# Performance work log

Hardware: AMD Instinct MI355X
Metric: run time of the kernel (lower is better)

The kernel has to match this reference:

```python
import jax, jax.numpy as jnp
import numpy as np

GRID_SIZE = 8
SPLINE_ORDER = 3  # cubic B-splines
GRID_MIN, GRID_MAX = -1.0, 1.0


def _make_grid():
    # Extended knot vector: grid_size + 2*order intervals -> G+2k+1 knots
    h = (GRID_MAX - GRID_MIN) / GRID_SIZE
    n = GRID_SIZE + 2 * SPLINE_ORDER + 1
    return jnp.asarray(GRID_MIN - SPLINE_ORDER * h + h * np.arange(n, dtype=np.float32))


def bspline_basis(x, grid, k):
    # x: (B, in) -> (B, in, G+k) via Cox-de Boor recursion
    x = x[..., None]
    b = ((x >= grid[:-1]) & (x < grid[1:])).astype(x.dtype)
    for p in range(1, k + 1):
        left = (x - grid[: -(p + 1)]) / (grid[p:-1] - grid[: -(p + 1)]) * b[..., :-1]
        right = (grid[p + 1:] - x) / (grid[p + 1:] - grid[1:-p]) * b[..., 1:]
        b = left + right
    return b


def setup_inputs() -> dict:
    key = jax.random.key(0)
    k1, k2, k3 = jax.random.split(key, 3)
    B, IN, OUT = 32768, 256, 256
    NB = GRID_SIZE + SPLINE_ORDER  # 11
    x = jax.random.normal(k1, (B, IN), dtype=jnp.float32)
    ln_gamma = jnp.ones((IN,), dtype=jnp.float32)
    ln_beta = jnp.zeros((IN,), dtype=jnp.float32)
    coeff = jax.random.normal(k2, (OUT, IN, NB), dtype=jnp.float32) * 0.1
    base_w = jax.random.normal(k3, (OUT, IN), dtype=jnp.float32) * (1.0 / np.sqrt(IN))
    return {"x": x, "ln_gamma": ln_gamma, "ln_beta": ln_beta, "coeff": coeff, "base_w": base_w}


def reference(x, ln_gamma, ln_beta, coeff, base_w):
    grid = _make_grid()
    # LayerNorm over in_features (eps = torch default 1e-5)
    mu = jnp.mean(x, axis=-1, keepdims=True)
    var = jnp.mean(jnp.square(x - mu), axis=-1, keepdims=True)
    normalized = (x - mu) * jax.lax.rsqrt(var + 1e-5) * ln_gamma + ln_beta
    # Spline branch: basis expansion (B, in, nb) contracted with coeff (out, in, nb)
    basis = bspline_basis(normalized, grid, SPLINE_ORDER)
    spline = jnp.einsum('bin,oin->bo', basis, coeff)
    # Base branch: SiLU(x) @ W^T (note: uses raw x, not normalized)
    base = jnp.einsum('bi,oi->bo', jax.nn.silu(x), base_w)
    return spline + base
```

## Files before the change

kernel.cpp:

```cpp
#include <hip/hip_runtime.h>
#include <hip/hip_bf16.h>

typedef _Float16 f16x8 __attribute__((ext_vector_type(8)));
typedef float f32x4 __attribute__((ext_vector_type(4)));

#define BM 128
#define NCHUNK 32
#define IN_F 256
#define OUT_F 256
#define KDIM 3072

__device__ inline void async_b16(const void* g, void* l) {
  __builtin_amdgcn_global_load_lds(
      (const __attribute__((address_space(1))) unsigned int*)g,
      (__attribute__((address_space(3))) unsigned int*)l, 16, 0, 0);
}

static __device__ inline unsigned pack2(float a, float b) {
  union { _Float16 h[2]; unsigned u; } t;
  t.h[0] = (_Float16)a;
  t.h[1] = (_Float16)b;
  return t.u;
}

__global__ __launch_bounds__(256) void prep_w(const float* __restrict__ coeff,
                                              const float* __restrict__ base_w,
                                              _Float16* __restrict__ W2F) {
  const int u   = blockIdx.x * 256 + threadIdx.x;
  const int c   = u / 3072;
  const int r   = u % 3072;
  const int bcb = r / 192;
  const int r2  = r % 192;
  const int g   = r2 / 64;
  const int ln  = r2 % 64;
  const int o   = bcb * 16 + (ln & 15);
  const int k8  = g * 4 + (ln >> 4);
  const int kh0 = c * 96 + k8 * 8;
  _Float16 h[8];
  #pragma unroll
  for (int e = 0; e < 8; ++e) {
    const int k = kh0 + e;
    const int i = k / 12, m = k % 12;
    const float v = (m == 11) ? base_w[o * IN_F + i] : coeff[(o * IN_F + i) * 11 + m];
    h[e] = (_Float16)v;
  }
  *(f16x8*)&W2F[(size_t)u * 8] = *(const f16x8*)h;
}

__global__ __launch_bounds__(1024, 4) void kan_fused(const float* __restrict__ x,
                                                     const float* __restrict__ gamma,
                                                     const float* __restrict__ beta,
                                                     const _Float16* __restrict__ W2F,
                                                     float* __restrict__ out) {
  __shared__ _Float16 A0[24 * 512], A1[24 * 512];
  __shared__ _Float16 B0[48 * 512], B1[48 * 512];
  __shared__ float mu_s[BM], rs_s[BM];

  const int tid  = threadIdx.x;
  const int lane = tid & 63;
  const int wid  = tid >> 6;
  const int row0 = blockIdx.x * BM;

  for (int rr = wid; rr < BM; rr += 16) {
    const float4 v = *(const float4*)(x + (size_t)(row0 + rr) * IN_F + lane * 4);
    float s  = v.x + v.y + v.z + v.w;
    float sq = v.x * v.x + v.y * v.y + v.z * v.z + v.w * v.w;
    #pragma unroll
    for (int off = 32; off >= 1; off >>= 1) {
      s  += __shfl_xor(s, off);
      sq += __shfl_xor(sq, off);
    }
    if (lane == 0) {
      const float mu  = s * (1.0f / 256.0f);
      const float var = sq * (1.0f / 256.0f) - mu * mu;
      mu_s[rr] = mu;
      rs_s[rr] = 1.0f / sqrtf(var + 1e-5f);
    }
  }
  __syncthreads();

  const bool isprod = (wid < 8);

  const int wr   = (wid >> 2) & 1;
  const int wc   = wid & 3;
  const int lrow = lane & 15;

  f32x4 acc[4][4] = {};

  const int plrow = tid & 15;
  const int pfq   = (tid >> 4) & 3;
  const int prb   = (tid >> 6) & 7;
  const int prow  = prb * 16 + plrow;
  const float mu = mu_s[prow], rs = rs_s[prow];
  const float* xrow = x + (size_t)(row0 + prow) * IN_F + pfq * 2;
  const float* grow = gamma + pfq * 2;
  const float* brow = beta + pfq * 2;

  int aoff0, aoff1, aoff2;
  {
    const int k80 = pfq * 3 + 0, k81 = pfq * 3 + 1, k82 = pfq * 3 + 2;
    aoff0 = (prb * 3 + (k80 >> 2)) * 512 + (k80 & 3) * 128 + plrow * 8;
    aoff1 = (prb * 3 + (k81 >> 2)) * 512 + (k81 & 3) * 128 + plrow * 8;
    aoff2 = (prb * 3 + (k82 >> 2)) * 512 + (k82 & 3) * 128 + plrow * 8;
  }

  const char* const wsrc = (const char*)W2F + (size_t)(wid & 7) * 6144 + (size_t)lane * 16;
  auto stageB = [&](int c, _Float16* Bb) {
    const char* gb = wsrc + (size_t)c * 49152;
    char* lb = (char*)Bb + (wid & 7) * 6144;
    #pragma unroll
    for (int j = 0; j < 6; ++j)
      async_b16(gb + j * 1024, lb + j * 1024);
  };

  auto produce = [&](_Float16* buf, float2 xv, float2 gv, float2 bv) {
    unsigned R[12];
    #pragma unroll
    for (int q = 0; q < 2; ++q) {
      const float xr = q ? xv.y : xv.x;
      const float gq = q ? gv.y : gv.x;
      const float bq = q ? bv.y : bv.x;
      const float n  = (xr - mu) * rs * gq + bq;
      const float v  = (n + 1.75f) * 4.0f;
      const float fj = floorf(v);
      const float u  = v - fj;
      const float u2 = u * u, u3 = u2 * u;
      const float w0 = (1.0f / 6.0f) * (1.0f - 3.0f * u + 3.0f * u2 - u3);
      const float w1 = (1.0f / 6.0f) * (3.0f * u3 - 6.0f * u2 + 4.0f);
      const float w2 = (1.0f / 6.0f) * (-3.0f * u3 + 3.0f * u2 + 3.0f * u + 1.0f);
      const float w3 = (1.0f / 6.0f) * u3;
      const unsigned W0 = pack2(w0, w1);
      const unsigned W1 = pack2(w2, w3);
      const int p    = (int)fj - 3;
      const bool odd = (p & 1);
      const unsigned v0 = odd ? (W0 << 16) : W0;
      const unsigned v1 = odd ? ((W0 >> 16) | (W1 << 16)) : W1;
      const unsigned v2 = odd ? (W1 >> 16) : 0u;
      const int s0 = (v >= 0.0f && v < 14.0f) ? (p >> 1) : 99;
      const int s1 = s0 + 1, s2 = s0 + 2;
      #pragma unroll
      for (int k = 0; k < 6; ++k) {
        unsigned r = (k == s0) ? v0 : 0u;
        r = (k == s1) ? v1 : r;
        r = (k == s2) ? v2 : r;
        R[q * 6 + k] = r;
      }
      const float sl = xr * __builtin_amdgcn_rcpf(1.0f + __expf(-xr));
      R[q * 6 + 5] = (R[q * 6 + 5] & 0x0000FFFFu) | pack2(0.0f, sl);
    }
    *(f16x8*)&buf[aoff0] = *(const f16x8*)&R[0];
    *(f16x8*)&buf[aoff1] = *(const f16x8*)&R[4];
    *(f16x8*)&buf[aoff2] = *(const f16x8*)&R[8];
  };

  auto domfma = [&](const _Float16* Ab, const _Float16* Bb) {
    #pragma unroll
    for (int fk = 0; fk < 3; ++fk) {
      f16x8 a[4], b[4];
      #pragma unroll
      for (int fm = 0; fm < 4; ++fm)
        a[fm] = *(const f16x8*)&Ab[((wr * 4 + fm) * 3 + fk) * 512 + lane * 8];
      #pragma unroll
      for (int fn = 0; fn < 4; ++fn)
        b[fn] = *(const f16x8*)&Bb[((wc * 4 + fn) * 3 + fk) * 512 + lane * 8];
      #pragma unroll
      for (int fm = 0; fm < 4; ++fm)
        #pragma unroll
        for (int fn = 0; fn < 4; ++fn)
          acc[fm][fn] = __builtin_amdgcn_mfma_f32_16x16x32_f16(a[fm], b[fn], acc[fm][fn], 0, 0, 0);
    }
  };

  float2 xv0 = {}, gv0 = {}, bv0 = {}, xv1 = {}, gv1 = {}, bv1 = {};
  if (isprod) {
    stageB(0, B0);
    xv0 = *(const float2*)(xrow);
    gv0 = *(const float2*)(grow);
    bv0 = *(const float2*)(brow);
    xv1 = *(const float2*)(xrow + 8);
    gv1 = *(const float2*)(grow + 8);
    bv1 = *(const float2*)(brow + 8);
    produce(A0, xv0, gv0, bv0);
  }
  __syncthreads();

  for (int c = 0; c < NCHUNK; c += 2) {
    const int cp2 = (c + 2 < NCHUNK) ? (c + 2) : (NCHUNK - 1);
    const int cp3 = (c + 3 < NCHUNK) ? (c + 3) : (NCHUNK - 1);
    if (isprod) {
      stageB(c + 1, B1);
      xv0 = *(const float2*)(xrow + cp2 * 8);
      gv0 = *(const float2*)(grow + cp2 * 8);
      bv0 = *(const float2*)(brow + cp2 * 8);
      produce(A1, xv1, gv1, bv1);
    } else {
      domfma(A0, B0);
    }
    __syncthreads();
    if (isprod) {
      if (c + 2 < NCHUNK) {
        stageB(cp2, B0);
        xv1 = *(const float2*)(xrow + cp3 * 8);
        gv1 = *(const float2*)(grow + cp3 * 8);
        bv1 = *(const float2*)(brow + cp3 * 8);
        produce(A0, xv0, gv0, bv0);
      }
    } else {
      domfma(A1, B1);
    }
    __syncthreads();
  }

  if (!isprod) {
    const int orow0 = row0 + wr * 64 + (lane >> 4) * 4;
    const int ocol0 = wc * 64 + lrow;
    #pragma unroll
    for (int fm = 0; fm < 4; ++fm)
      #pragma unroll
      for (int fn = 0; fn < 4; ++fn)
        #pragma unroll
        for (int r = 0; r < 4; ++r)
          out[(size_t)(orow0 + fm * 16 + r) * OUT_F + ocol0 + fn * 16] = acc[fm][fn][r];
  }
}

extern "C" void kernel_launch(void* const* d_in, const int* in_sizes, int n_in,
                              void* d_out, int out_size, void* d_ws, size_t ws_size,
                              hipStream_t stream) {
  const float* x      = (const float*)d_in[0];
  const float* gamma  = (const float*)d_in[1];
  const float* beta   = (const float*)d_in[2];
  const float* coeff  = (const float*)d_in[3];
  const float* base_w = (const float*)d_in[4];
  float* out = (float*)d_out;
  _Float16* W2F = (_Float16*)d_ws;

  prep_w<<<dim3(384), dim3(256), 0, stream>>>(coeff, base_w, W2F);
  kan_fused<<<dim3(32768 / BM), dim3(1024), 0, stream>>>(x, gamma, beta, W2F, out);
}
```

Measured before the change: 74.04 us.

## Load weight fragments directly from global into registers instead of LDS staging

Removes the LDS double buffers for the weight matrix and the async global-to-LDS copies. Consumer waves now load their B fragments straight from global memory (L2) into registers, software-pipelined one k-step ahead. This frees LDS and removes producer-side staging work, but each consumer wave now issues redundant global loads, since the two row-group waves fetch the same columns. Load latency is exposed to the MFMA loop and is only covered by the single-step prefetch.

```diff
diff --git a/kernel.cpp b/kernel.cpp
--- a/kernel.cpp
+++ b/kernel.cpp
@@ -9,12 +9,6 @@
 #define IN_F 256
 #define OUT_F 256
 #define KDIM 3072
-
-__device__ inline void async_b16(const void* g, void* l) {
-  __builtin_amdgcn_global_load_lds(
-      (const __attribute__((address_space(1))) unsigned int*)g,
-      (__attribute__((address_space(3))) unsigned int*)l, 16, 0, 0);
-}
 
 static __device__ inline unsigned pack2(float a, float b) {
   union { _Float16 h[2]; unsigned u; } t;
@@ -53,7 +47,6 @@
                                                      const _Float16* __restrict__ W2F,
                                                      float* __restrict__ out) {
   __shared__ _Float16 A0[24 * 512], A1[24 * 512];
-  __shared__ _Float16 B0[48 * 512], B1[48 * 512];
   __shared__ float mu_s[BM], rs_s[BM];
 
   const int tid  = threadIdx.x;
@@ -103,15 +96,6 @@
     aoff1 = (prb * 3 + (k81 >> 2)) * 512 + (k81 & 3) * 128 + plrow * 8;
     aoff2 = (prb * 3 + (k82 >> 2)) * 512 + (k82 & 3) * 128 + plrow * 8;
   }
-
-  const char* const wsrc = (const char*)W2F + (size_t)(wid & 7) * 6144 + (size_t)lane * 16;
-  auto stageB = [&](int c, _Float16* Bb) {
-    const char* gb = wsrc + (size_t)c * 49152;
-    char* lb = (char*)Bb + (wid & 7) * 6144;
-    #pragma unroll
-    for (int j = 0; j < 6; ++j)
-      async_b16(gb + j * 1024, lb + j * 1024);
-  };
 
   auto produce = [&](_Float16* buf, float2 xv, float2 gv, float2 bv) {
     unsigned R[12];
@@ -153,27 +137,30 @@
     *(f16x8*)&buf[aoff2] = *(const f16x8*)&R[8];
   };
 
-  auto domfma = [&](const _Float16* Ab, const _Float16* Bb) {
-    #pragma unroll
-    for (int fk = 0; fk < 3; ++fk) {
-      f16x8 a[4], b[4];
-      #pragma unroll
-      for (int fm = 0; fm < 4; ++fm)
-        a[fm] = *(const f16x8*)&Ab[((wr * 4 + fm) * 3 + fk) * 512 + lane * 8];
+  const char* const wbsrc = (const char*)W2F + (size_t)wc * 12288 + (size_t)lane * 16;
+  auto loadB4 = [&](int c, int fk, f16x8* b4) {
+    const char* gb = wbsrc + (size_t)c * 49152;
+    #pragma unroll
+    for (int fn = 0; fn < 4; ++fn)
+      b4[fn] = *(const f16x8*)(gb + (fn * 3 + fk) * 1024);
+  };
+  auto constage = [&](const _Float16* Ab, int fk, const f16x8* bcur,
+                      f16x8* bnx, int cl, int fkl) {
+    loadB4(cl, fkl, bnx);
+    f16x8 a[4];
+    #pragma unroll
+    for (int fm = 0; fm < 4; ++fm)
+      a[fm] = *(const f16x8*)&Ab[((wr * 4 + fm) * 3 + fk) * 512 + lane * 8];
+    #pragma unroll
+    for (int fm = 0; fm < 4; ++fm)
       #pragma unroll
       for (int fn = 0; fn < 4; ++fn)
-        b[fn] = *(const f16x8*)&Bb[((wc * 4 + fn) * 3 + fk) * 512 + lane * 8];
-      #pragma unroll
-      for (int fm = 0; fm < 4; ++fm)
-        #pragma unroll
-        for (int fn = 0; fn < 4; ++fn)
-          acc[fm][fn] = __builtin_amdgcn_mfma_f32_16x16x32_f16(a[fm], b[fn], acc[fm][fn], 0, 0, 0);
-    }
+        acc[fm][fn] = __builtin_amdgcn_mfma_f32_16x16x32_f16(a[fm], bcur[fn], acc[fm][fn], 0, 0, 0);
   };
 
   float2 xv0 = {}, gv0 = {}, bv0 = {}, xv1 = {}, gv1 = {}, bv1 = {};
+  f16x8 bX[4], bY[4];
   if (isprod) {
-    stageB(0, B0);
     xv0 = *(const float2*)(xrow);
     gv0 = *(const float2*)(grow);
     bv0 = *(const float2*)(brow);
@@ -181,32 +168,38 @@
     gv1 = *(const float2*)(grow + 8);
     bv1 = *(const float2*)(brow + 8);
     produce(A0, xv0, gv0, bv0);
+  } else {
+    loadB4(0, 0, bX);
   }
   __syncthreads();
 
   for (int c = 0; c < NCHUNK; c += 2) {
-    const int cp2 = (c + 2 < NCHUNK) ? (c + 2) : (NCHUNK - 1);
+    const int cn1 = (c + 1 < NCHUNK) ? (c + 1) : (NCHUNK - 1);
+    const int cn2 = (c + 2 < NCHUNK) ? (c + 2) : (NCHUNK - 1);
+    const int cp2 = cn2;
     const int cp3 = (c + 3 < NCHUNK) ? (c + 3) : (NCHUNK - 1);
     if (isprod) {
-      stageB(c + 1, B1);
       xv0 = *(const float2*)(xrow + cp2 * 8);
       gv0 = *(const float2*)(grow + cp2 * 8);
       bv0 = *(const float2*)(brow + cp2 * 8);
       produce(A1, xv1, gv1, bv1);
     } else {
-      domfma(A0, B0);
+      constage(A0, 0, bX, bY, c, 1);
+      constage(A0, 1, bY, bX, c, 2);
+      constage(A0, 2, bX, bY, cn1, 0);
     }
     __syncthreads();
     if (isprod) {
       if (c + 2 < NCHUNK) {
-        stageB(cp2, B0);
         xv1 = *(const float2*)(xrow + cp3 * 8);
         gv1 = *(const float2*)(grow + cp3 * 8);
         bv1 = *(const float2*)(brow + cp3 * 8);
         produce(A0, xv0, gv0, bv0);
       }
     } else {
-      domfma(A1, B1);
+      constage(A1, 0, bY, bX, c + 1, 1);
+      constage(A1, 1, bX, bY, c + 1, 2);
+      constage(A1, 2, bY, bX, cn2, 0);
     }
     __syncthreads();
   }
```

After: 116.8 us. 1.58x slower.

## Switch GEMM to 32x32x16 MFMA tiles with matching A/B LDS layouts

Applied to the files above, without the earlier changes.

Replaces the 16x16x32 f16 MFMA tiling (4x4 accumulators per wave) with 32x32x16 MFMA (2x2 accumulators of 16 floats). The weight prep kernel and the producer's A-tile LDS write offsets are reorganized to match the 32-row fragment layout, and the epilogue is rewritten for the new accumulator mapping. The aim is fewer LDS fragment loads per MFMA and better reuse per instruction. In exchange, the producer now writes A with split 8-byte stores, which may cause more LDS bank conflicts.

```diff
diff --git a/kernel.cpp b/kernel.cpp
--- a/kernel.cpp
+++ b/kernel.cpp
@@ -2,7 +2,8 @@
 #include <hip/hip_bf16.h>
 
 typedef _Float16 f16x8 __attribute__((ext_vector_type(8)));
-typedef float f32x4 __attribute__((ext_vector_type(4)));
+typedef float f32x16 __attribute__((ext_vector_type(16)));
+typedef unsigned u32x2 __attribute__((ext_vector_type(2)));
 
 #define BM 128
 #define NCHUNK 32
@@ -29,13 +30,12 @@
   const int u   = blockIdx.x * 256 + threadIdx.x;
   const int c   = u / 3072;
   const int r   = u % 3072;
-  const int bcb = r / 192;
-  const int r2  = r % 192;
-  const int g   = r2 / 64;
+  const int cb  = r / 384;
+  const int r2  = r % 384;
+  const int kg  = r2 / 64;
   const int ln  = r2 % 64;
-  const int o   = bcb * 16 + (ln & 15);
-  const int k8  = g * 4 + (ln >> 4);
-  const int kh0 = c * 96 + k8 * 8;
+  const int o   = cb * 32 + (ln & 31);
+  const int kh0 = c * 96 + kg * 16 + (ln >> 5) * 8;
   _Float16 h[8];
   #pragma unroll
   for (int e = 0; e < 8; ++e) {
@@ -61,8 +61,8 @@
   const int wid  = tid >> 6;
   const int row0 = blockIdx.x * BM;
 
-  for (int rr = wid; rr < BM; rr += 16) {
-    const float4 v = *(const float4*)(x + (size_t)(row0 + rr) * IN_F + lane * 4);
+  for (int rr0 = wid; rr0 < BM; rr0 += 16) {
+    const float4 v = *(const float4*)(x + (size_t)(row0 + rr0) * IN_F + lane * 4);
     float s  = v.x + v.y + v.z + v.w;
     float sq = v.x * v.x + v.y * v.y + v.z * v.z + v.w * v.w;
     #pragma unroll
@@ -73,8 +73,8 @@
     if (lane == 0) {
       const float mu  = s * (1.0f / 256.0f);
       const float var = sq * (1.0f / 256.0f) - mu * mu;
-      mu_s[rr] = mu;
-      rs_s[rr] = 1.0f / sqrtf(var + 1e-5f);
+      mu_s[rr0] = mu;
+      rs_s[rr0] = 1.0f / sqrtf(var + 1e-5f);
     }
   }
   __syncthreads();
@@ -83,9 +83,8 @@
 
   const int wr   = (wid >> 2) & 1;
   const int wc   = wid & 3;
-  const int lrow = lane & 15;
-
-  f32x4 acc[4][4] = {};
+
+  f32x16 acc[2][2] = {};
 
   const int plrow = tid & 15;
   const int pfq   = (tid >> 4) & 3;
@@ -96,12 +95,15 @@
   const float* grow = gamma + pfq * 2;
   const float* brow = beta + pfq * 2;
 
-  int aoff0, aoff1, aoff2;
+  const int rb  = prow >> 5, rr = prow & 31;
+  const int base3 = (pfq >> 1) * 3;
+  int o1, o2, o3, o4;
   {
-    const int k80 = pfq * 3 + 0, k81 = pfq * 3 + 1, k82 = pfq * 3 + 2;
-    aoff0 = (prb * 3 + (k80 >> 2)) * 512 + (k80 & 3) * 128 + plrow * 8;
-    aoff1 = (prb * 3 + (k81 >> 2)) * 512 + (k81 & 3) * 128 + plrow * 8;
-    aoff2 = (prb * 3 + (k82 >> 2)) * 512 + (k82 & 3) * 128 + plrow * 8;
+    const int g0 = (rb * 6 + base3) * 512 + rr * 8;
+    const int g1 = (rb * 6 + base3 + 1) * 512 + rr * 8;
+    const int g2 = (rb * 6 + base3 + 2) * 512 + rr * 8;
+    if (!(pfq & 1)) { o1 = g0; o2 = g0 + 256; o3 = o2 + 4; o4 = g1; }
+    else            { o1 = g1 + 256; o2 = g2; o3 = o2 + 4; o4 = g2 + 256; }
   }
 
   const char* const wsrc = (const char*)W2F + (size_t)(wid & 7) * 6144 + (size_t)lane * 16;
@@ -148,26 +150,27 @@
       const float sl = xr * __builtin_amdgcn_rcpf(1.0f + __expf(-xr));
       R[q * 6 + 5] = (R[q * 6 + 5] & 0x0000FFFFu) | pack2(0.0f, sl);
     }
-    *(f16x8*)&buf[aoff0] = *(const f16x8*)&R[0];
-    *(f16x8*)&buf[aoff1] = *(const f16x8*)&R[4];
-    *(f16x8*)&buf[aoff2] = *(const f16x8*)&R[8];
+    *(f16x8*)&buf[o1] = *(const f16x8*)&R[0];
+    *(u32x2*)&buf[o2] = *(const u32x2*)&R[4];
+    *(u32x2*)&buf[o3] = *(const u32x2*)&R[6];
+    *(f16x8*)&buf[o4] = *(const f16x8*)&R[8];
   };
 
   auto domfma = [&](const _Float16* Ab, const _Float16* Bb) {
     #pragma unroll
-    for (int fk = 0; fk < 3; ++fk) {
-      f16x8 a[4], b[4];
-      #pragma unroll
-      for (int fm = 0; fm < 4; ++fm)
-        a[fm] = *(const f16x8*)&Ab[((wr * 4 + fm) * 3 + fk) * 512 + lane * 8];
-      #pragma unroll
-      for (int fn = 0; fn < 4; ++fn)
-        b[fn] = *(const f16x8*)&Bb[((wc * 4 + fn) * 3 + fk) * 512 + lane * 8];
-      #pragma unroll
-      for (int fm = 0; fm < 4; ++fm)
+    for (int kg = 0; kg < 6; ++kg) {
+      f16x8 a[2], b[2];
+      #pragma unroll
+      for (int tr = 0; tr < 2; ++tr)
+        a[tr] = *(const f16x8*)&Ab[((2 * wr + tr) * 6 + kg) * 512 + lane * 8];
+      #pragma unroll
+      for (int tc = 0; tc < 2; ++tc)
+        b[tc] = *(const f16x8*)&Bb[((2 * wc + tc) * 6 + kg) * 512 + lane * 8];
+      #pragma unroll
+      for (int tr = 0; tr < 2; ++tr)
         #pragma unroll
-        for (int fn = 0; fn < 4; ++fn)
-          acc[fm][fn] = __builtin_amdgcn_mfma_f32_16x16x32_f16(a[fm], b[fn], acc[fm][fn], 0, 0, 0);
+        for (int tc = 0; tc < 2; ++tc)
+          acc[tr][tc] = __builtin_amdgcn_mfma_f32_32x32x16_f16(a[tr], b[tc], acc[tr][tc], 0, 0, 0);
     }
   };
 
@@ -212,15 +215,16 @@
   }
 
   if (!isprod) {
-    const int orow0 = row0 + wr * 64 + (lane >> 4) * 4;
-    const int ocol0 = wc * 64 + lrow;
-    #pragma unroll
-    for (int fm = 0; fm < 4; ++fm)
-      #pragma unroll
-      for (int fn = 0; fn < 4; ++fn)
+    #pragma unroll
+    for (int tr = 0; tr < 2; ++tr)
+      #pragma unroll
+      for (int tc = 0; tc < 2; ++tc) {
+        const int orow_b = row0 + wr * 64 + tr * 32 + 4 * (lane >> 5);
+        const int ocol   = wc * 64 + tc * 32 + (lane & 31);
         #pragma unroll
-        for (int r = 0; r < 4; ++r)
-          out[(size_t)(orow0 + fm * 16 + r) * OUT_F + ocol0 + fn * 16] = acc[fm][fn][r];
+        for (int r = 0; r < 16; ++r)
+          out[(size_t)(orow_b + (r & 3) + 8 * (r >> 2)) * OUT_F + ocol] = acc[tr][tc][r];
+      }
   }
 }
 
```

Measured after the change: 81.49 us. 1.1x slower.
